# Optimization experiments

Measured on AMD Instinct MI355X. Metric: run time of the kernel, lower is better.

## Reference

```python
import jax, jax.numpy as jnp
import numpy as np

N = 100_000   # num nodes
E = 1_000_000 # num edges
F = 64        # feat_dim
H = 64        # hidden_dim
D = 64        # embed_dim


def _xavier(key, shape):
    limit = float(np.sqrt(6.0 / (shape[0] + shape[1])))
    return jax.random.uniform(key, shape, jnp.float32, -limit, limit)


def setup_inputs() -> dict:
    key = jax.random.key(0)
    ks = jax.random.split(key, 8)
    x = jax.random.normal(ks[0], (N, F), jnp.float32)
    edge_index = jax.random.randint(ks[1], (2, E), 0, N, dtype=jnp.int64)
    # GCNConv weights stored [in, out] (torch Linear transposed); biases zero-init
    return {
        "x": x,
        "edge_index": edge_index,
        "W1": _xavier(ks[2], (F, H)), "b1": jnp.zeros((H,), jnp.float32),
        "W2": _xavier(ks[3], (H, H)), "b2": jnp.zeros((H,), jnp.float32),
        "W3": _xavier(ks[4], (H, D)), "b3": jnp.zeros((D,), jnp.float32),
        "fw1": _xavier(ks[5], (D, H)), "fb1": jnp.zeros((H,), jnp.float32),
        "fw2": _xavier(ks[6], (H, D)), "fb2": jnp.zeros((D,), jnp.float32),
    }


def _gcn_conv(x, src, dst, dinv, W, b):
    # GCNConv: out = D^{-1/2} (A+I) D^{-1/2} (x W) + b
    h = x @ W                                   # [N, out]
    norm = dinv[src] * dinv[dst]                # [E]
    msg = h[src] * norm[:, None]                # gather + scale: [E, out]
    agg = jax.ops.segment_sum(msg, dst, num_segments=N)
    agg = agg + h * (dinv * dinv)[:, None]      # self-loop term
    return agg + b


def reference(x, edge_index, W1, b1, W2, b2, W3, b3, fw1, fb1, fw2, fb2):
    src, dst = edge_index[0], edge_index[1]
    # degree with self-loops (symmetric normalization)
    deg = jax.ops.segment_sum(jnp.ones((E,), x.dtype), dst, num_segments=N) + 1.0
    dinv = jax.lax.rsqrt(deg)
    # eval mode: dropout(p=0.5, training=False) is identity
    h = jax.nn.relu(_gcn_conv(x, src, dst, dinv, W1, b1))
    h = jax.nn.relu(_gcn_conv(h, src, dst, dinv, W2, b2))
    h = jax.nn.relu(_gcn_conv(h, src, dst, dinv, W3, b3))
    h = jax.nn.relu(h @ fw1 + fb1)
    return h @ fw2 + fb2                        # node embeddings [N, D]
```

## Files before the change

### kernel.cpp

```cpp
#include <hip/hip_runtime.h>
#include <cstdint>
#include <cstddef>


#define CDIV(a, b) (((a) + (b) - 1) / (b))

typedef __attribute__((ext_vector_type(8))) short bf16x8;
typedef __attribute__((ext_vector_type(4))) float f32x4;

static constexpr int BKT_SHIFT = 10;
static constexpr int BKT_NODES = 1 << BKT_SHIFT;
static constexpr int BKT_CAP = 13312;

__device__ __forceinline__ void split_bf(float a, short& hi, short& lo) {
  unsigned u = __float_as_uint(a);
  unsigned r = u + (0x7FFF + ((u >> 16) & 1));
  hi = (short)(r >> 16);
  float hirec = __uint_as_float(r & 0xFFFF0000u);
  float res = a - hirec;
  lo = (short)(__float_as_uint(res) >> 16);
}

__device__ __forceinline__ unsigned short f2bf_rne(float a) {
  unsigned u = __float_as_uint(a);
  u += 0x7FFF + ((u >> 16) & 1);
  return (unsigned short)(u >> 16);
}

__device__ __forceinline__ void split8(float4 x, float4 y, bf16x8& h, bf16x8& l) {
  float av[8] = {x.x, x.y, x.z, x.w, y.x, y.y, y.z, y.w};
#pragma unroll
  for (int j = 0; j < 8; ++j) {
    short hi, lo;
    split_bf(av[j], hi, lo);
    h[j] = hi;
    l[j] = lo;
  }
}

__device__ __forceinline__ float4 nt_ld4(const float* p) {
  f32x4 v = __builtin_nontemporal_load(reinterpret_cast<const f32x4*>(p));
  float4 r;
  r.x = v[0]; r.y = v[1]; r.z = v[2]; r.w = v[3];
  return r;
}

__global__ __launch_bounds__(256)
void k_bucket(const int* __restrict__ ei, int* __restrict__ bcnt,
              int2* __restrict__ pairs, int E) {
  __shared__ int hist[128], rbase[128], roff[128];
  int t = threadIdx.x;
  int chunk = (E + gridDim.x - 1) / gridDim.x;
  int e0 = blockIdx.x * chunk;
  int e1 = min(e0 + chunk, E);
  if (t < 128) hist[t] = 0;
  __syncthreads();
  for (int e = e0 + t; e < e1; e += 256) {
    int d = __builtin_nontemporal_load(&ei[E + e]);
    atomicAdd(&hist[d >> BKT_SHIFT], 1);
  }
  __syncthreads();
  if (t < 128) {
    roff[t] = 0;
    rbase[t] = hist[t] ? atomicAdd(&bcnt[t], hist[t]) : 0;
  }
  __syncthreads();
  for (int e = e0 + t; e < e1; e += 256) {
    int d = __builtin_nontemporal_load(&ei[E + e]);
    int s = __builtin_nontemporal_load(&ei[e]);
    int b = d >> BKT_SHIFT;
    int r = atomicAdd(&roff[b], 1);
    int idx = rbase[b] + r;
    if (idx < BKT_CAP) pairs[(size_t)b * BKT_CAP + idx] = make_int2(s, d);
  }
}

__global__ __launch_bounds__(1024)
void k_build(const int2* __restrict__ pairs, const int* __restrict__ bcnt,
             int* __restrict__ row_ptr, float* __restrict__ dinv,
             int* __restrict__ srcs, int N, int E, int K) {
  __shared__ int cnt[BKT_NODES];
  __shared__ int deg[BKT_NODES];
  __shared__ int ebase_sh;
  int b = blockIdx.x;
  int t = threadIdx.x;
  int lo = b << BKT_SHIFT;
  int range = min(BKT_NODES, N - lo);
  int sz = min(bcnt[b], BKT_CAP);
  if (t == 0) {
    int s = 0;
    for (int i = 0; i < b; ++i) s += bcnt[i];
    ebase_sh = s;
  }
  cnt[t] = 0;
  __syncthreads();
  int ebase = ebase_sh;
  const int2* pb = pairs + (size_t)b * BKT_CAP;
  for (int i = t; i < sz; i += 1024) {
    atomicAdd(&cnt[pb[i].y - lo], 1);
  }
  __syncthreads();
  deg[t] = cnt[t];
  __syncthreads();
  int offset = 1;
  for (int d2 = BKT_NODES / 2; d2 > 0; d2 >>= 1) {
    if (t < d2) {
      int ai = offset * (2 * t + 1) - 1;
      int bi = offset * (2 * t + 2) - 1;
      cnt[bi] += cnt[ai];
    }
    offset <<= 1;
    __syncthreads();
  }
  if (t == 0) cnt[BKT_NODES - 1] = 0;
  __syncthreads();
  for (int d2 = 1; d2 < BKT_NODES; d2 <<= 1) {
    offset >>= 1;
    if (t < d2) {
      int ai = offset * (2 * t + 1) - 1;
      int bi = offset * (2 * t + 2) - 1;
      int tmp = cnt[ai];
      cnt[ai] = cnt[bi];
      cnt[bi] += tmp;
    }
    __syncthreads();
  }
  if (t < range) {
    row_ptr[lo + t] = ebase + cnt[t];
    dinv[lo + t] = rsqrtf((float)deg[t] + 1.0f);
  }
  if (b == K - 1 && t == 0) row_ptr[N] = E;
  __syncthreads();
  for (int i = t; i < sz; i += 1024) {
    int2 p = pb[i];
    int pos = ebase + atomicAdd(&cnt[p.y - lo], 1);
    srcs[pos] = p.x;
  }
}

__global__ void k_prep(const float* __restrict__ w0, const float* __restrict__ w1,
                       const float* __restrict__ w2, const float* __restrict__ w3,
                       const float* __restrict__ w4, bf16x8* __restrict__ packed,
                       int* __restrict__ bcnt) {
  if (blockIdx.x == 5) {
    if (threadIdx.x < 128) bcnt[threadIdx.x] = 0;
    return;
  }
  const float* W;
  switch (blockIdx.x) {
    case 0: W = w0; break;
    case 1: W = w1; break;
    case 2: W = w2; break;
    case 3: W = w3; break;
    default: W = w4; break;
  }
  int tid = threadIdx.x;
  int lane = tid & 63;
  int q = (tid >> 6) & 1;
  int t = tid >> 7;
  int col = lane & 15, quad = lane >> 4;
  bf16x8 hi8, lo8;
#pragma unroll
  for (int j = 0; j < 8; ++j) {
    int k = q * 32 + quad * 8 + j;
    short hi, lo;
    split_bf(W[k * 64 + t * 16 + col], hi, lo);
    hi8[j] = hi;
    lo8[j] = lo;
  }
  size_t base = (size_t)blockIdx.x * 1024 + ((t * 2 + q) * 2) * 64 + lane;
  packed[base] = hi8;
  packed[base + 64] = lo8;
}

__global__ __launch_bounds__(256, 4)
void k_mm(const float* __restrict__ in, const bf16x8* __restrict__ Wp,
          const float* __restrict__ dinv, unsigned short* __restrict__ out, int n) {
  if (blockIdx.x == 0 && threadIdx.x < 32) {
    ((unsigned int*)out)[(size_t)n * 32 + threadIdx.x] = 0u;
  }
  int lane = threadIdx.x & 63;
  int col = lane & 15, quad = lane >> 4;
  int tile = (blockIdx.x * blockDim.x + threadIdx.x) >> 6;
  int ntiles = (n + 15) >> 4;
  if (tile >= ntiles) return;

  bf16x8 wh[4][2], wl[4][2];
#pragma unroll
  for (int t = 0; t < 4; ++t)
#pragma unroll
    for (int q = 0; q < 2; ++q) {
      wh[t][q] = Wp[((t * 2 + q) * 2) * 64 + lane];
      wl[t][q] = Wp[((t * 2 + q) * 2 + 1) * 64 + lane];
    }

  int row0 = tile << 4;
  int ar = row0 + col;
  if (ar > n - 1) ar = n - 1;
  const float* arow = in + (size_t)ar * 64 + quad * 8;
  float4 a0 = nt_ld4(arow), a1 = nt_ld4(arow + 4);
  float4 a2 = nt_ld4(arow + 32), a3 = nt_ld4(arow + 36);

  bf16x8 ah[2], al[2];
  split8(a0, a1, ah[0], al[0]);
  split8(a2, a3, ah[1], al[1]);

  f32x4 acc[4];
#pragma unroll
  for (int t = 0; t < 4; ++t) acc[t] = (f32x4){0.f, 0.f, 0.f, 0.f};
#pragma unroll
  for (int t = 0; t < 4; ++t)
#pragma unroll
    for (int q = 0; q < 2; ++q) {
      acc[t] = __builtin_amdgcn_mfma_f32_16x16x32_bf16(ah[q], wh[t][q], acc[t], 0, 0, 0);
      acc[t] = __builtin_amdgcn_mfma_f32_16x16x32_bf16(ah[q], wl[t][q], acc[t], 0, 0, 0);
      acc[t] = __builtin_amdgcn_mfma_f32_16x16x32_bf16(al[q], wh[t][q], acc[t], 0, 0, 0);
    }
  float dv[4];
#pragma unroll
  for (int r = 0; r < 4; ++r) {
    int row = row0 + quad * 4 + r;
    dv[r] = (row < n) ? dinv[row] : 0.0f;
  }
#pragma unroll
  for (int t = 0; t < 4; ++t)
#pragma unroll
    for (int r = 0; r < 4; ++r) {
      int row = row0 + quad * 4 + r;
      if (row < n) out[(size_t)row * 64 + t * 16 + col] = f2bf_rne(acc[t][r] * dv[r]);
    }
}

template <bool HEAD>
__global__ __launch_bounds__(256, 4)
void k_agg_mm(const unsigned short* __restrict__ hws, const float* __restrict__ dinv,
              const int* __restrict__ row_ptr, const int* __restrict__ srcs,
              const float* __restrict__ bagg,
              const bf16x8* __restrict__ Wp1, const float* __restrict__ b1p,
              const bf16x8* __restrict__ Wp2, const float* __restrict__ b2p,
              void* __restrict__ out, int n) {
  constexpr int LDP = 68;
  __shared__ float a_sh[32 * LDP];
  int tid = threadIdx.x;
  int g = tid >> 3;
  int fg = tid & 7;
  int row0 = blockIdx.x << 5;
  const uint4* hw4 = (const uint4*)hws;

  if (!HEAD && blockIdx.x == 0 && tid < 32) {
    ((unsigned int*)out)[(size_t)n * 32 + tid] = 0u;
  }

  int node = row0 + g;
  bool valid = node < n;
  int nd = valid ? node : n;
  uint4 su = hw4[(size_t)nd * 8 + fg];
  float di = valid ? dinv[node] : 0.f;
  int p0 = 0, p1 = 0;
  if (valid) {
    p0 = row_ptr[node];
    p1 = row_ptr[node + 1];
  }
  float acc[8] = {0.f, 0.f, 0.f, 0.f, 0.f, 0.f, 0.f, 0.f};
  if (p0 < p1) {
    int s[8];
#pragma unroll
    for (int j = 0; j < 8; ++j) {
      int ij = p0 + j;
      bool ok = ij < p1;
      int sv = __builtin_nontemporal_load(&srcs[ok ? ij : p1 - 1]);
      s[j] = ok ? sv : n;
    }
    for (int p = p0; p < p1; p += 8) {
      uint4 u[8];
#pragma unroll
      for (int j = 0; j < 8; ++j) u[j] = hw4[(size_t)s[j] * 8 + fg];
      int pn = p + 8;
      if (pn < p1) {
#pragma unroll
        for (int j = 0; j < 8; ++j) {
          int ij = pn + j;
          bool ok = ij < p1;
          int sv = __builtin_nontemporal_load(&srcs[ok ? ij : p1 - 1]);
          s[j] = ok ? sv : n;
        }
      }
#pragma unroll
      for (int j = 0; j < 8; ++j) {
        acc[0] += __uint_as_float(u[j].x << 16);
        acc[1] += __uint_as_float(u[j].x & 0xFFFF0000u);
        acc[2] += __uint_as_float(u[j].y << 16);
        acc[3] += __uint_as_float(u[j].y & 0xFFFF0000u);
        acc[4] += __uint_as_float(u[j].z << 16);
        acc[5] += __uint_as_float(u[j].z & 0xFFFF0000u);
        acc[6] += __uint_as_float(u[j].w << 16);
        acc[7] += __uint_as_float(u[j].w & 0xFFFF0000u);
      }
    }
  }
  {
    float sf[8];
    sf[0] = __uint_as_float(su.x << 16);
    sf[1] = __uint_as_float(su.x & 0xFFFF0000u);
    sf[2] = __uint_as_float(su.y << 16);
    sf[3] = __uint_as_float(su.y & 0xFFFF0000u);
    sf[4] = __uint_as_float(su.z << 16);
    sf[5] = __uint_as_float(su.z & 0xFFFF0000u);
    sf[6] = __uint_as_float(su.w << 16);
    sf[7] = __uint_as_float(su.w & 0xFFFF0000u);
    float r[8];
#pragma unroll
    for (int k = 0; k < 8; ++k) {
      float bk = bagg[fg * 8 + k];
      r[k] = valid ? fmaxf(fmaf(di, acc[k] + sf[k], bk), 0.f) : 0.f;
    }
    float* dst = &a_sh[g * LDP + (fg << 3)];
    *(float4*)(dst) = make_float4(r[0], r[1], r[2], r[3]);
    *(float4*)(dst + 4) = make_float4(r[4], r[5], r[6], r[7]);
  }
  __syncthreads();

  int lane = tid & 63;
  int wave = tid >> 6;
  int col = lane & 15, quad = lane >> 4;

  bf16x8 wh[2], wl[2];
#pragma unroll
  for (int q = 0; q < 2; ++q) {
    wh[q] = Wp1[((wave * 2 + q) * 2) * 64 + lane];
    wl[q] = Wp1[((wave * 2 + q) * 2 + 1) * 64 + lane];
  }
  f32x4 acc1[2];
#pragma unroll
  for (int rt = 0; rt < 2; ++rt) {
    const float* arow = &a_sh[(rt * 16 + col) * LDP + (quad << 3)];
    float4 a0 = *(const float4*)(arow);
    float4 a1 = *(const float4*)(arow + 4);
    float4 a2 = *(const float4*)(arow + 32);
    float4 a3 = *(const float4*)(arow + 36);
    bf16x8 ah[2], al[2];
    split8(a0, a1, ah[0], al[0]);
    split8(a2, a3, ah[1], al[1]);
    acc1[rt] = (f32x4){0.f, 0.f, 0.f, 0.f};
#pragma unroll
    for (int q = 0; q < 2; ++q) {
      acc1[rt] = __builtin_amdgcn_mfma_f32_16x16x32_bf16(ah[q], wh[q], acc1[rt], 0, 0, 0);
      acc1[rt] = __builtin_amdgcn_mfma_f32_16x16x32_bf16(ah[q], wl[q], acc1[rt], 0, 0, 0);
      acc1[rt] = __builtin_amdgcn_mfma_f32_16x16x32_bf16(al[q], wh[q], acc1[rt], 0, 0, 0);
    }
  }

  if constexpr (!HEAD) {
#pragma unroll
    for (int rt = 0; rt < 2; ++rt)
#pragma unroll
      for (int r = 0; r < 4; ++r) {
        int row = row0 + rt * 16 + (quad << 2) + r;
        if (row < n) {
          ((unsigned short*)out)[(size_t)row * 64 + wave * 16 + col] =
              f2bf_rne(acc1[rt][r] * dinv[row]);
        }
      }
  } else {
    __shared__ float h_sh[32 * LDP];
    float bv1 = b1p[wave * 16 + col];
#pragma unroll
    for (int rt = 0; rt < 2; ++rt)
#pragma unroll
      for (int r = 0; r < 4; ++r) {
        h_sh[(rt * 16 + (quad << 2) + r) * LDP + wave * 16 + col] =
            fmaxf(acc1[rt][r] + bv1, 0.f);
      }
    __syncthreads();
    bf16x8 wh2[2], wl2[2];
#pragma unroll
    for (int q = 0; q < 2; ++q) {
      wh2[q] = Wp2[((wave * 2 + q) * 2) * 64 + lane];
      wl2[q] = Wp2[((wave * 2 + q) * 2 + 1) * 64 + lane];
    }
    float bv2 = b2p[wave * 16 + col];
#pragma unroll
    for (int rt = 0; rt < 2; ++rt) {
      const float* hrow = &h_sh[(rt * 16 + col) * LDP + (quad << 3)];
      float4 h0 = *(const float4*)(hrow);
      float4 h1 = *(const float4*)(hrow + 4);
      float4 h2 = *(const float4*)(hrow + 32);
      float4 h3 = *(const float4*)(hrow + 36);
      bf16x8 ah2[2], al2[2];
      split8(h0, h1, ah2[0], al2[0]);
      split8(h2, h3, ah2[1], al2[1]);
      f32x4 acc2 = (f32x4){0.f, 0.f, 0.f, 0.f};
#pragma unroll
      for (int q = 0; q < 2; ++q) {
        acc2 = __builtin_amdgcn_mfma_f32_16x16x32_bf16(ah2[q], wh2[q], acc2, 0, 0, 0);
        acc2 = __builtin_amdgcn_mfma_f32_16x16x32_bf16(ah2[q], wl2[q], acc2, 0, 0, 0);
        acc2 = __builtin_amdgcn_mfma_f32_16x16x32_bf16(al2[q], wh2[q], acc2, 0, 0, 0);
      }
#pragma unroll
      for (int r = 0; r < 4; ++r) {
        int row = row0 + rt * 16 + (quad << 2) + r;
        if (row < n) {
          ((float*)out)[(size_t)row * 64 + wave * 16 + col] = acc2[r] + bv2;
        }
      }
    }
  }
}

extern "C" void kernel_launch(void* const* d_in, const int* in_sizes, int n_in,
                              void* d_out, int out_size, void* d_ws, size_t ws_size,
                              hipStream_t stream) {
  const float* x = (const float*)d_in[0];
  const int* ei = (const int*)d_in[1];
  const float* W1 = (const float*)d_in[2];
  const float* b1 = (const float*)d_in[3];
  const float* W2 = (const float*)d_in[4];
  const float* b2 = (const float*)d_in[5];
  const float* W3 = (const float*)d_in[6];
  const float* b3 = (const float*)d_in[7];
  const float* fw1 = (const float*)d_in[8];
  const float* fb1 = (const float*)d_in[9];
  const float* fw2 = (const float*)d_in[10];
  const float* fb2 = (const float*)d_in[11];
  float* out = (float*)d_out;

  const int N = in_sizes[0] / 64;
  const int E = in_sizes[1] / 2;
  const int K = CDIV(N, BKT_NODES);

  char* w = (char*)d_ws;
  auto take = [&](size_t bytes) -> char* {
    char* p = w;
    w += (bytes + 255) & ~(size_t)255;
    return p;
  };
  float* dinv = (float*)take((size_t)N * 4);
  int* row_ptr = (int*)take((size_t)(N + 1) * 4);
  int* bcnt = (int*)take((size_t)128 * 4);
  int* srcs = (int*)take((size_t)E * 4);
  bf16x8* wpack = (bf16x8*)take((size_t)5 * 1024 * 16);
  unsigned short* hwsA = (unsigned short*)take((size_t)(N + 1) * 64 * 2);
  unsigned short* hwsB = (unsigned short*)take((size_t)(N + 1) * 64 * 2);
  int2* pairs = (int2*)hwsA;

  const int B = 256;

  k_prep<<<6, 512, 0, stream>>>(W1, W2, W3, fw1, fw2, wpack, bcnt);
  k_bucket<<<1024, B, 0, stream>>>(ei, bcnt, pairs, E);
  k_build<<<K, 1024, 0, stream>>>(pairs, bcnt, row_ptr, dinv, srcs, N, E, K);

  const int ntiles16 = CDIV(N, 16);
  const int MMG = CDIV(ntiles16, 4);
  const int ntiles32 = CDIV(N, 32);

  k_mm<<<MMG, B, 0, stream>>>(x, wpack + 0 * 1024, dinv, hwsA, N);
  k_agg_mm<false><<<ntiles32, B, 0, stream>>>(hwsA, dinv, row_ptr, srcs, b1,
                                              wpack + 1 * 1024, nullptr, nullptr, nullptr,
                                              hwsB, N);
  k_agg_mm<false><<<ntiles32, B, 0, stream>>>(hwsB, dinv, row_ptr, srcs, b2,
                                              wpack + 2 * 1024, nullptr, nullptr, nullptr,
                                              hwsA, N);
  k_agg_mm<true><<<ntiles32, B, 0, stream>>>(hwsA, dinv, row_ptr, srcs, b3,
                                             wpack + 3 * 1024, fb1, wpack + 4 * 1024, fb2,
                                             out, N);
}
```

Baseline: 271.2 us.

## Halve CSR bucket size, raise aggregation occupancy, share LDS tile in head

The CSR build now uses 512-node buckets instead of 1024, which doubles the number of k_build blocks. k_bucket runs on half as many blocks with 256-entry histograms. The aggregation kernel drops its software-prefetched source-index pipeline for a simpler per-chunk loop and raises the launch-bounds occupancy hint from 4 to 6 blocks. In the head variant the second LDS tile is gone and a_sh is reused behind an extra barrier, which reduces shared memory and register pressure. The cost is less latency hiding on the index loads, and k_build still launches 1024-thread blocks for 512-node buckets, so half of each block sits idle.

```diff
diff --git a/kernel.cpp b/kernel.cpp
--- a/kernel.cpp
+++ b/kernel.cpp
@@ -8,9 +8,9 @@
 typedef __attribute__((ext_vector_type(8))) short bf16x8;
 typedef __attribute__((ext_vector_type(4))) float f32x4;
 
-static constexpr int BKT_SHIFT = 10;
+static constexpr int BKT_SHIFT = 9;
 static constexpr int BKT_NODES = 1 << BKT_SHIFT;
-static constexpr int BKT_CAP = 13312;
+static constexpr int BKT_CAP = 7424;
 
 __device__ __forceinline__ void split_bf(float a, short& hi, short& lo) {
   unsigned u = __float_as_uint(a);
@@ -27,6 +27,15 @@
   return (unsigned short)(u >> 16);
 }
 
+__device__ __forceinline__ float4 bf4_to_f4(uint2 u) {
+  float4 v;
+  v.x = __uint_as_float(u.x << 16);
+  v.y = __uint_as_float(u.x & 0xFFFF0000u);
+  v.z = __uint_as_float(u.y << 16);
+  v.w = __uint_as_float(u.y & 0xFFFF0000u);
+  return v;
+}
+
 __device__ __forceinline__ void split8(float4 x, float4 y, bf16x8& h, bf16x8& l) {
   float av[8] = {x.x, x.y, x.z, x.w, y.x, y.y, y.z, y.w};
 #pragma unroll
@@ -48,22 +57,20 @@
 __global__ __launch_bounds__(256)
 void k_bucket(const int* __restrict__ ei, int* __restrict__ bcnt,
               int2* __restrict__ pairs, int E) {
-  __shared__ int hist[128], rbase[128], roff[128];
+  __shared__ int hist[256], rbase[256], roff[256];
   int t = threadIdx.x;
   int chunk = (E + gridDim.x - 1) / gridDim.x;
   int e0 = blockIdx.x * chunk;
   int e1 = min(e0 + chunk, E);
-  if (t < 128) hist[t] = 0;
+  hist[t] = 0;
   __syncthreads();
   for (int e = e0 + t; e < e1; e += 256) {
     int d = __builtin_nontemporal_load(&ei[E + e]);
     atomicAdd(&hist[d >> BKT_SHIFT], 1);
   }
   __syncthreads();
-  if (t < 128) {
-    roff[t] = 0;
-    rbase[t] = hist[t] ? atomicAdd(&bcnt[t], hist[t]) : 0;
-  }
+  roff[t] = 0;
+  rbase[t] = hist[t] ? atomicAdd(&bcnt[t], hist[t]) : 0;
   __syncthreads();
   for (int e = e0 + t; e < e1; e += 256) {
     int d = __builtin_nontemporal_load(&ei[E + e]);
@@ -92,7 +99,7 @@
     for (int i = 0; i < b; ++i) s += bcnt[i];
     ebase_sh = s;
   }
-  cnt[t] = 0;
+  if (t < BKT_NODES) cnt[t] = 0;
   __syncthreads();
   int ebase = ebase_sh;
   const int2* pb = pairs + (size_t)b * BKT_CAP;
@@ -100,7 +107,7 @@
     atomicAdd(&cnt[pb[i].y - lo], 1);
   }
   __syncthreads();
-  deg[t] = cnt[t];
+  if (t < BKT_NODES) deg[t] = cnt[t];
   __syncthreads();
   int offset = 1;
   for (int d2 = BKT_NODES / 2; d2 > 0; d2 >>= 1) {
@@ -143,7 +150,7 @@
                        const float* __restrict__ w4, bf16x8* __restrict__ packed,
                        int* __restrict__ bcnt) {
   if (blockIdx.x == 5) {
-    if (threadIdx.x < 128) bcnt[threadIdx.x] = 0;
+    if (threadIdx.x < 256) bcnt[threadIdx.x] = 0;
     return;
   }
   const float* W;
@@ -176,8 +183,8 @@
 __global__ __launch_bounds__(256, 4)
 void k_mm(const float* __restrict__ in, const bf16x8* __restrict__ Wp,
           const float* __restrict__ dinv, unsigned short* __restrict__ out, int n) {
-  if (blockIdx.x == 0 && threadIdx.x < 32) {
-    ((unsigned int*)out)[(size_t)n * 32 + threadIdx.x] = 0u;
+  if (blockIdx.x == 0 && threadIdx.x < 64) {
+    out[(size_t)n * 64 + threadIdx.x] = 0;
   }
   int lane = threadIdx.x & 63;
   int col = lane & 15, quad = lane >> 4;
@@ -232,7 +239,7 @@
 }
 
 template <bool HEAD>
-__global__ __launch_bounds__(256, 4)
+__global__ __launch_bounds__(256, 6)
 void k_agg_mm(const unsigned short* __restrict__ hws, const float* __restrict__ dinv,
               const int* __restrict__ row_ptr, const int* __restrict__ srcs,
               const float* __restrict__ bagg,
@@ -243,18 +250,18 @@
   __shared__ float a_sh[32 * LDP];
   int tid = threadIdx.x;
   int g = tid >> 3;
-  int fg = tid & 7;
+  int q = tid & 7;
   int row0 = blockIdx.x << 5;
   const uint4* hw4 = (const uint4*)hws;
 
-  if (!HEAD && blockIdx.x == 0 && tid < 32) {
-    ((unsigned int*)out)[(size_t)n * 32 + tid] = 0u;
+  if (!HEAD && blockIdx.x == 0 && tid < 64) {
+    ((unsigned short*)out)[(size_t)n * 64 + tid] = 0;
   }
 
   int node = row0 + g;
   bool valid = node < n;
   int nd = valid ? node : n;
-  uint4 su = hw4[(size_t)nd * 8 + fg];
+  uint4 su = hw4[(size_t)nd * 8 + q];
   float di = valid ? dinv[node] : 0.f;
   int p0 = 0, p1 = 0;
   if (valid) {
@@ -262,40 +269,28 @@
     p1 = row_ptr[node + 1];
   }
   float acc[8] = {0.f, 0.f, 0.f, 0.f, 0.f, 0.f, 0.f, 0.f};
-  if (p0 < p1) {
+  for (int p = p0; p < p1; p += 8) {
     int s[8];
 #pragma unroll
     for (int j = 0; j < 8; ++j) {
-      int ij = p0 + j;
+      int ij = p + j;
       bool ok = ij < p1;
       int sv = __builtin_nontemporal_load(&srcs[ok ? ij : p1 - 1]);
       s[j] = ok ? sv : n;
     }
-    for (int p = p0; p < p1; p += 8) {
-      uint4 u[8];
-#pragma unroll
-      for (int j = 0; j < 8; ++j) u[j] = hw4[(size_t)s[j] * 8 + fg];
-      int pn = p + 8;
-      if (pn < p1) {
-#pragma unroll
-        for (int j = 0; j < 8; ++j) {
-          int ij = pn + j;
-          bool ok = ij < p1;
-          int sv = __builtin_nontemporal_load(&srcs[ok ? ij : p1 - 1]);
-          s[j] = ok ? sv : n;
-        }
-      }
-#pragma unroll
-      for (int j = 0; j < 8; ++j) {
-        acc[0] += __uint_as_float(u[j].x << 16);
-        acc[1] += __uint_as_float(u[j].x & 0xFFFF0000u);
-        acc[2] += __uint_as_float(u[j].y << 16);
-        acc[3] += __uint_as_float(u[j].y & 0xFFFF0000u);
-        acc[4] += __uint_as_float(u[j].z << 16);
-        acc[5] += __uint_as_float(u[j].z & 0xFFFF0000u);
-        acc[6] += __uint_as_float(u[j].w << 16);
-        acc[7] += __uint_as_float(u[j].w & 0xFFFF0000u);
-      }
+    uint4 u[8];
+#pragma unroll
+    for (int j = 0; j < 8; ++j) u[j] = hw4[(size_t)s[j] * 8 + q];
+#pragma unroll
+    for (int j = 0; j < 8; ++j) {
+      acc[0] += __uint_as_float(u[j].x << 16);
+      acc[1] += __uint_as_float(u[j].x & 0xFFFF0000u);
+      acc[2] += __uint_as_float(u[j].y << 16);
+      acc[3] += __uint_as_float(u[j].y & 0xFFFF0000u);
+      acc[4] += __uint_as_float(u[j].z << 16);
+      acc[5] += __uint_as_float(u[j].z & 0xFFFF0000u);
+      acc[6] += __uint_as_float(u[j].w << 16);
+      acc[7] += __uint_as_float(u[j].w & 0xFFFF0000u);
     }
   }
   {
@@ -311,10 +306,10 @@
     float r[8];
 #pragma unroll
     for (int k = 0; k < 8; ++k) {
-      float bk = bagg[fg * 8 + k];
+      float bk = bagg[q * 8 + k];
       r[k] = valid ? fmaxf(fmaf(di, acc[k] + sf[k], bk), 0.f) : 0.f;
     }
-    float* dst = &a_sh[g * LDP + (fg << 3)];
+    float* dst = &a_sh[g * LDP + (q << 3)];
     *(float4*)(dst) = make_float4(r[0], r[1], r[2], r[3]);
     *(float4*)(dst + 4) = make_float4(r[4], r[5], r[6], r[7]);
   }
@@ -326,9 +321,9 @@
 
   bf16x8 wh[2], wl[2];
 #pragma unroll
-  for (int q = 0; q < 2; ++q) {
-    wh[q] = Wp1[((wave * 2 + q) * 2) * 64 + lane];
-    wl[q] = Wp1[((wave * 2 + q) * 2 + 1) * 64 + lane];
+  for (int q2 = 0; q2 < 2; ++q2) {
+    wh[q2] = Wp1[((wave * 2 + q2) * 2) * 64 + lane];
+    wl[q2] = Wp1[((wave * 2 + q2) * 2 + 1) * 64 + lane];
   }
   f32x4 acc1[2];
 #pragma unroll
@@ -343,10 +338,10 @@
     split8(a2, a3, ah[1], al[1]);
     acc1[rt] = (f32x4){0.f, 0.f, 0.f, 0.f};
 #pragma unroll
-    for (int q = 0; q < 2; ++q) {
-      acc1[rt] = __builtin_amdgcn_mfma_f32_16x16x32_bf16(ah[q], wh[q], acc1[rt], 0, 0, 0);
-      acc1[rt] = __builtin_amdgcn_mfma_f32_16x16x32_bf16(ah[q], wl[q], acc1[rt], 0, 0, 0);
-      acc1[rt] = __builtin_amdgcn_mfma_f32_16x16x32_bf16(al[q], wh[q], acc1[rt], 0, 0, 0);
+    for (int q2 = 0; q2 < 2; ++q2) {
+      acc1[rt] = __builtin_amdgcn_mfma_f32_16x16x32_bf16(ah[q2], wh[q2], acc1[rt], 0, 0, 0);
+      acc1[rt] = __builtin_amdgcn_mfma_f32_16x16x32_bf16(ah[q2], wl[q2], acc1[rt], 0, 0, 0);
+      acc1[rt] = __builtin_amdgcn_mfma_f32_16x16x32_bf16(al[q2], wh[q2], acc1[rt], 0, 0, 0);
     }
   }
 
@@ -362,26 +357,26 @@
         }
       }
   } else {
-    __shared__ float h_sh[32 * LDP];
     float bv1 = b1p[wave * 16 + col];
+    __syncthreads();
 #pragma unroll
     for (int rt = 0; rt < 2; ++rt)
 #pragma unroll
       for (int r = 0; r < 4; ++r) {
-        h_sh[(rt * 16 + (quad << 2) + r) * LDP + wave * 16 + col] =
+        a_sh[(rt * 16 + (quad << 2) + r) * LDP + wave * 16 + col] =
             fmaxf(acc1[rt][r] + bv1, 0.f);
       }
     __syncthreads();
     bf16x8 wh2[2], wl2[2];
 #pragma unroll
-    for (int q = 0; q < 2; ++q) {
-      wh2[q] = Wp2[((wave * 2 + q) * 2) * 64 + lane];
-      wl2[q] = Wp2[((wave * 2 + q) * 2 + 1) * 64 + lane];
+    for (int q2 = 0; q2 < 2; ++q2) {
+      wh2[q2] = Wp2[((wave * 2 + q2) * 2) * 64 + lane];
+      wl2[q2] = Wp2[((wave * 2 + q2) * 2 + 1) * 64 + lane];
     }
     float bv2 = b2p[wave * 16 + col];
 #pragma unroll
     for (int rt = 0; rt < 2; ++rt) {
-      const float* hrow = &h_sh[(rt * 16 + col) * LDP + (quad << 3)];
+      const float* hrow = &a_sh[(rt * 16 + col) * LDP + (quad << 3)];
       float4 h0 = *(const float4*)(hrow);
       float4 h1 = *(const float4*)(hrow + 4);
       float4 h2 = *(const float4*)(hrow + 32);
@@ -391,10 +386,10 @@
       split8(h2, h3, ah2[1], al2[1]);
       f32x4 acc2 = (f32x4){0.f, 0.f, 0.f, 0.f};
 #pragma unroll
-      for (int q = 0; q < 2; ++q) {
-        acc2 = __builtin_amdgcn_mfma_f32_16x16x32_bf16(ah2[q], wh2[q], acc2, 0, 0, 0);
-        acc2 = __builtin_amdgcn_mfma_f32_16x16x32_bf16(ah2[q], wl2[q], acc2, 0, 0, 0);
-        acc2 = __builtin_amdgcn_mfma_f32_16x16x32_bf16(al2[q], wh2[q], acc2, 0, 0, 0);
+      for (int q2 = 0; q2 < 2; ++q2) {
+        acc2 = __builtin_amdgcn_mfma_f32_16x16x32_bf16(ah2[q2], wh2[q2], acc2, 0, 0, 0);
+        acc2 = __builtin_amdgcn_mfma_f32_16x16x32_bf16(ah2[q2], wl2[q2], acc2, 0, 0, 0);
+        acc2 = __builtin_amdgcn_mfma_f32_16x16x32_bf16(al2[q2], wh2[q2], acc2, 0, 0, 0);
       }
 #pragma unroll
       for (int r = 0; r < 4; ++r) {
@@ -436,7 +431,7 @@
   };
   float* dinv = (float*)take((size_t)N * 4);
   int* row_ptr = (int*)take((size_t)(N + 1) * 4);
-  int* bcnt = (int*)take((size_t)128 * 4);
+  int* bcnt = (int*)take((size_t)256 * 4);
   int* srcs = (int*)take((size_t)E * 4);
   bf16x8* wpack = (bf16x8*)take((size_t)5 * 1024 * 16);
   unsigned short* hwsA = (unsigned short*)take((size_t)(N + 1) * 64 * 2);
@@ -446,7 +441,7 @@
   const int B = 256;
 
   k_prep<<<6, 512, 0, stream>>>(W1, W2, W3, fw1, fw2, wpack, bcnt);
-  k_bucket<<<1024, B, 0, stream>>>(ei, bcnt, pairs, E);
+  k_bucket<<<512, B, 0, stream>>>(ei, bcnt, pairs, E);
   k_build<<<K, 1024, 0, stream>>>(pairs, bcnt, row_ptr, dinv, srcs, N, E, K);
 
   const int ntiles16 = CDIV(N, 16);
```

After: 247.5 us. 8.8% less time.
